# Kernel tuning notes

Hardware: AMD Instinct MI355X
Metric: run time of the kernel (lower is better)

## Reference

```python
import jax, jax.numpy as jnp
import numpy as np

RRELU_SLOPE = (1.0 / 8.0 + 1.0 / 3.0) / 2.0  # F.rrelu eval-mode slope = 11/48

N_NODES = 50000
N_EDGES = 800000
H_DIM = 128
N_REL2 = 460  # 2 * num_rels
T_DIM = 64
BATCH = 1024
SEQ_LEN = 10


def _rrelu(x):
    return jnp.where(x >= 0, x, x * RRELU_SLOPE)


def _rgcn_layer(h, rel, src, dst, etype, norm, has_in, w_neigh, loop_w, evolve_w):
    # UnionRGCNLayer (comp='sub'): msg = (h_src - rel[etype]) @ W_neigh, sum into dst, * 1/indeg
    msg = (h[src] - rel[etype]) @ w_neigh                                # [E, h]
    agg = jax.ops.segment_sum(msg, dst, num_segments=h.shape[0]) * norm  # [N, h]
    # self-loop: nodes with in-degree>0 use loop_weight, isolated nodes use evolve_loop_weight
    loop_msg = jnp.where(has_in[:, None], h @ loop_w, h @ evolve_w)
    return _rrelu(agg + loop_msg)  # dropout p=0.0 -> identity


def setup_inputs() -> dict:
    key = jax.random.key(0)
    ks = jax.random.split(key, 12)
    sc = 1.0 / np.sqrt(H_DIM)
    return {
        "h": jax.random.normal(ks[0], (N_NODES, H_DIM), jnp.float32),
        "rel_embeds": jax.random.normal(ks[1], (N_REL2, H_DIM), jnp.float32),
        "w_neigh1": jax.random.normal(ks[2], (H_DIM, H_DIM), jnp.float32) * sc,
        "loop_w1": jax.random.normal(ks[3], (H_DIM, H_DIM), jnp.float32) * sc,
        "evolve_w1": jax.random.normal(ks[4], (H_DIM, H_DIM), jnp.float32) * sc,
        "w_neigh2": jax.random.normal(ks[5], (H_DIM, H_DIM), jnp.float32) * sc,
        "loop_w2": jax.random.normal(ks[6], (H_DIM, H_DIM), jnp.float32) * sc,
        "evolve_w2": jax.random.normal(ks[7], (H_DIM, H_DIM), jnp.float32) * sc,
        "t_w": jax.random.normal(ks[8], (T_DIM,), jnp.float32),
        "t_b": jax.random.normal(ks[9], (T_DIM,), jnp.float32),
        "src": jax.random.randint(ks[10], (N_EDGES,), 0, N_NODES, jnp.int32),
        "dst": jax.random.randint(ks[11], (N_EDGES,), 0, N_NODES, jnp.int32),
        "etype": jax.random.randint(jax.random.fold_in(key, 1), (N_EDGES,), 0, N_REL2, jnp.int32),
        "node_ids_graph": jax.random.randint(jax.random.fold_in(key, 2), (BATCH, SEQ_LEN), 0, N_NODES + 1, jnp.int32),
        "times": jax.random.randint(jax.random.fold_in(key, 3), (BATCH, SEQ_LEN), 0, 1000, jnp.int32),
    }


def reference(h, rel_embeds, w_neigh1, loop_w1, evolve_w1, w_neigh2, loop_w2, evolve_w2,
              t_w, t_b, src, dst, etype, node_ids_graph, times):
    N, H = h.shape
    deg = jax.ops.segment_sum(jnp.ones_like(dst, dtype=h.dtype), dst, num_segments=N)
    has_in = deg > 0
    norm = (1.0 / jnp.maximum(deg, 1.0))[:, None]  # dgl 'norm' = 1/in-degree

    h1 = _rgcn_layer(h, rel_embeds, src, dst, etype, norm, has_in, w_neigh1, loop_w1, evolve_w1)
    h2 = _rgcn_layer(h1, rel_embeds, src, dst, etype, norm, has_in, w_neigh2, loop_w2, evolve_w2)

    # concat zero padding row, then irregular gather by node_ids_graph
    embeds = jnp.concatenate([h2, jnp.zeros((1, H), h.dtype)], axis=0)  # [N+1, h]
    s_embed = embeds[node_ids_graph]                                    # [B, L, h]

    B, L = node_ids_graph.shape
    t = times.reshape(-1, 1).astype(h.dtype)                            # [B*L, 1]
    time_emb = jnp.cos(t * t_w + t_b).reshape(B, L, t_w.shape[0])       # [B, L, t_dim]

    return jnp.concatenate([s_embed, time_emb], axis=-1)  # dropout p=0.0 -> identity
```

## Files before the change

kernel.cpp:

```cpp
#include <hip/hip_runtime.h>


#define HD 128
#define TD 64
#define BSH 7
#define NBLK 256
constexpr float SLOPE = 11.0f / 48.0f;

typedef unsigned short u16;
typedef unsigned int u32;
typedef short bf16x8 __attribute__((ext_vector_type(8)));
typedef float f32x4 __attribute__((ext_vector_type(4)));

__device__ __forceinline__ float bf2f(u16 b) {
    return __uint_as_float(((u32)b) << 16);
}
__device__ __forceinline__ u16 f2bf(float f) {
    u32 u = __float_as_uint(f);
    u += 0x7FFFu + ((u >> 16) & 1u);
    return (u16)(u >> 16);
}

__global__ __launch_bounds__(256)
void conv_kernel(const float4* __restrict__ in, ushort4* __restrict__ out, int n4)
{
    int i = blockIdx.x * 256 + threadIdx.x;
    if (i >= n4) return;
    float4 v = in[i];
    ushort4 o;
    o.x = f2bf(v.x); o.y = f2bf(v.y); o.z = f2bf(v.z); o.w = f2bf(v.w);
    out[i] = o;
}

__global__ __launch_bounds__(256)
void bt_kernel(const float* __restrict__ Wn, const float* __restrict__ Lw,
               u16* __restrict__ BT)
{
    int idx = blockIdx.x * 256 + threadIdx.x;
    int c = idx >> 8, k = idx & 255;
    float v = (k < HD) ? Wn[k * HD + c] : Lw[(k - HD) * HD + c];
    BT[(size_t)c * 256 + k] = f2bf(v);
}

__global__ __launch_bounds__(256)
void cntA(const int* __restrict__ dst, int E, int* __restrict__ cnt, int NBKT)
{
    __shared__ int hist[512];
    const int b = blockIdx.x, t = threadIdx.x;
    for (int i = t; i < NBKT; i += 256) hist[i] = 0;
    __syncthreads();
    const int chunk = (E + NBLK - 1) / NBLK;
    const int e0 = b * chunk;
    const int e1 = (e0 + chunk < E) ? e0 + chunk : E;
    for (int e = e0 + t; e < e1; e += 256)
        atomicAdd(&hist[dst[e] >> BSH], 1);
    __syncthreads();
    for (int i = t; i < NBKT; i += 256)
        cnt[(size_t)i * NBLK + b] = hist[i];
}

__global__ __launch_bounds__(256)
void scan1_kernel(const int* __restrict__ v, int* __restrict__ bsum, int M)
{
    __shared__ int red[256];
    const int b = blockIdx.x, t = threadIdx.x;
    int s = 0;
    #pragma unroll
    for (int j = 0; j < 4; j++) {
        int i = b * 1024 + j * 256 + t;
        if (i < M) s += v[i];
    }
    red[t] = s;
    __syncthreads();
    for (int off = 128; off; off >>= 1) {
        if (t < off) red[t] += red[t + off];
        __syncthreads();
    }
    if (t == 0) bsum[b] = red[0];
}

__global__ __launch_bounds__(64)
void scan2_kernel(int* __restrict__ bsum, int NB, int* __restrict__ totalOut)
{
    if (threadIdx.x == 0 && blockIdx.x == 0) {
        int acc = 0;
        for (int b = 0; b < NB; b++) { int x = bsum[b]; bsum[b] = acc; acc += x; }
        *totalOut = acc;
    }
}

__global__ __launch_bounds__(1024)
void scan3_kernel(const int* __restrict__ v, const int* __restrict__ bsum,
                  int* __restrict__ start, int M)
{
    __shared__ int buf[1024];
    const int b = blockIdx.x, t = threadIdx.x;
    const int i = b * 1024 + t;
    const int x = (i < M) ? v[i] : 0;
    buf[t] = x;
    __syncthreads();
    for (int off = 1; off < 1024; off <<= 1) {
        int y = (t >= off) ? buf[t - off] : 0;
        __syncthreads();
        buf[t] += y;
        __syncthreads();
    }
    if (i < M) start[i] = bsum[b] + buf[t] - x;
}

__global__ __launch_bounds__(256)
void passA2(const int* __restrict__ src, const int* __restrict__ dst,
            const int* __restrict__ ety, const int* __restrict__ start,
            u32* __restrict__ elistA, int E, int NBKT)
{
    __shared__ int cur[512];
    const int b = blockIdx.x, t = threadIdx.x;
    for (int i = t; i < NBKT; i += 256) cur[i] = start[(size_t)i * NBLK + b];
    __syncthreads();
    const int chunk = (E + NBLK - 1) / NBLK;
    const int e0 = b * chunk;
    const int e1 = (e0 + chunk < E) ? e0 + chunk : E;
    for (int e = e0 + t; e < e1; e += 256) {
        int d = dst[e];
        u32 entry = ((u32)(d & 127) << 25) | ((u32)ety[e] << 16) | (u32)src[e];
        int pos = atomicAdd(&cur[d >> BSH], 1);
        elistA[pos] = entry;
    }
}

__global__ __launch_bounds__(256)
void passB(const u32* __restrict__ elistA, const int* __restrict__ start,
           u32* __restrict__ elist, int* __restrict__ rowstart, int Nn, int E,
           int NBKT)
{
    __shared__ int cnt[128];
    __shared__ int ofs[128];
    const int b = blockIdx.x, t = threadIdx.x;
    const int beg = start[(size_t)b * NBLK];
    const int end = (b + 1 < NBKT) ? start[(size_t)(b + 1) * NBLK] : E;
    if (t < 128) cnt[t] = 0;
    __syncthreads();
    for (int i = beg + t; i < end; i += 256)
        atomicAdd(&cnt[elistA[i] >> 25], 1);
    __syncthreads();
    if (t == 0) {
        int acc = 0;
        for (int j = 0; j < 128; j++) { ofs[j] = acc; acc += cnt[j]; }
    }
    __syncthreads();
    const int n0 = b << BSH;
    if (t < 128 && n0 + t < Nn) rowstart[n0 + t] = beg + ofs[t];
    if (b == 0 && t == 0) rowstart[Nn] = E;
    __syncthreads();
    for (int i = beg + t; i < end; i += 256) {
        u32 v = elistA[i];
        int p = atomicAdd(&ofs[v >> 25], 1);
        elist[beg + p] = v & 0x01ffffffu;
    }
}

__global__ __launch_bounds__(64)
void gagg_kernel(const u32* __restrict__ hbf2, const u32* __restrict__ relbf2,
                 const u32* __restrict__ elist, const int* __restrict__ rowstart,
                 u32* __restrict__ Sn2, int Nn)
{
    int n = blockIdx.x;
    if (n >= Nn) return;
    int c = threadIdx.x;
    int beg = rowstart[n], end = rowstart[n + 1];
    float ae[8] = {}, ao[8] = {};
    int i = beg;
    for (; i + 8 <= end; i += 8) {
        #pragma unroll
        for (int j = 0; j < 8; j++) {
            u32 v = elist[i + j];
            u32 hv = hbf2[(size_t)(v & 0xffffu) * 64 + c];
            u32 rv = relbf2[(size_t)(v >> 16) * 64 + c];
            ae[j] += bf2f((u16)(hv & 0xffffu)) - bf2f((u16)(rv & 0xffffu));
            ao[j] += bf2f((u16)(hv >> 16)) - bf2f((u16)(rv >> 16));
        }
    }
    for (; i < end; i++) {
        u32 v = elist[i];
        u32 hv = hbf2[(size_t)(v & 0xffffu) * 64 + c];
        u32 rv = relbf2[(size_t)(v >> 16) * 64 + c];
        ae[0] += bf2f((u16)(hv & 0xffffu)) - bf2f((u16)(rv & 0xffffu));
        ao[0] += bf2f((u16)(hv >> 16)) - bf2f((u16)(rv >> 16));
    }
    float se = ((ae[0] + ae[1]) + (ae[2] + ae[3])) + ((ae[4] + ae[5]) + (ae[6] + ae[7]));
    float so = ((ao[0] + ao[1]) + (ao[2] + ao[3])) + ((ao[4] + ao[5]) + (ao[6] + ao[7]));
    int d = end - beg;
    float nrm = 1.0f / (float)((d > 0) ? d : 1);
    se *= nrm; so *= nrm;
    Sn2[(size_t)n * 64 + c] = (u32)f2bf(se) | ((u32)f2bf(so) << 16);
}

template<int STORE_BF16>
__global__ __launch_bounds__(256)
void mfma_kernel(const u16* __restrict__ Sn, const u16* __restrict__ Hn,
                 const u16* __restrict__ BT, const int* __restrict__ rowstart,
                 const float* __restrict__ Ew, void* __restrict__ Out, int Nn)
{
    const int lane = threadIdx.x & 63;
    const int wave = threadIdx.x >> 6;
    const int row0 = blockIdx.x * 128 + wave * 32;
    const int lr = lane & 15;
    const int lk = (lane >> 4) * 8;

    f32x4 acc[2][8];
    #pragma unroll
    for (int m = 0; m < 2; m++)
        #pragma unroll
        for (int n = 0; n < 8; n++)
            acc[m][n] = (f32x4){0.f, 0.f, 0.f, 0.f};

    int r0 = row0 + lr;      if (r0 >= Nn) r0 = Nn - 1;
    int r1 = row0 + 16 + lr; if (r1 >= Nn) r1 = Nn - 1;
    const size_t rb0 = (size_t)r0 * HD, rb1 = (size_t)r1 * HD;

    #pragma unroll
    for (int ks = 0; ks < 8; ks++) {
        const u16* A = (ks < 4) ? Sn : Hn;
        const int kc = (ks & 3) * 32 + lk;
        bf16x8 a0 = *(const bf16x8*)&A[rb0 + kc];
        bf16x8 a1 = *(const bf16x8*)&A[rb1 + kc];
        #pragma unroll
        for (int nf = 0; nf < 8; nf++) {
            bf16x8 b = *(const bf16x8*)&BT[(size_t)(nf * 16 + lr) * 256 + ks * 32 + lk];
            acc[0][nf] = __builtin_amdgcn_mfma_f32_16x16x32_bf16(a0, b, acc[0][nf], 0, 0, 0);
            acc[1][nf] = __builtin_amdgcn_mfma_f32_16x16x32_bf16(a1, b, acc[1][nf], 0, 0, 0);
        }
    }

    #pragma unroll
    for (int mf = 0; mf < 2; mf++) {
        #pragma unroll
        for (int r = 0; r < 4; r++) {
            const int row = row0 + mf * 16 + (lane >> 4) * 4 + r;
            if (row >= Nn) continue;
            const int d = rowstart[row + 1] - rowstart[row];
            #pragma unroll
            for (int nf = 0; nf < 8; nf++) {
                const int col = nf * 16 + lr;
                float o = acc[mf][nf][r];
                if (d == 0) {
                    o = 0.f;
                    for (int k = 0; k < HD; k++)
                        o = fmaf(bf2f(Hn[(size_t)row * HD + k]), Ew[(size_t)k * HD + col], o);
                }
                o = (o >= 0.f) ? o : o * SLOPE;
                if (STORE_BF16) ((u16*)Out)[(size_t)row * HD + col] = f2bf(o);
                else            ((float*)Out)[(size_t)row * HD + col] = o;
            }
        }
    }
}

__global__ __launch_bounds__(192)
void out_kernel(const float* __restrict__ h2, const int* __restrict__ ids,
                const int* __restrict__ tms,
                const float* __restrict__ tw, const float* __restrict__ tb,
                float* __restrict__ out, int R, int Nn)
{
    int r = blockIdx.x;
    int c = threadIdx.x;
    if (r >= R) return;
    float v;
    if (c < HD) {
        int id = ids[r];
        v = (id >= 0 && id < Nn) ? h2[(size_t)id * HD + c] : 0.0f;
    } else {
        int j = c - HD;
        v = cosf((float)tms[r] * tw[j] + tb[j]);
    }
    out[(size_t)r * (HD + TD) + c] = v;
}

extern "C" void kernel_launch(void* const* d_in, const int* in_sizes, int n_in,
                              void* d_out, int out_size, void* d_ws, size_t ws_size,
                              hipStream_t stream)
{
    const float* h   = (const float*)d_in[0];
    const float* rel = (const float*)d_in[1];
    const float* wn1 = (const float*)d_in[2];
    const float* lw1 = (const float*)d_in[3];
    const float* ew1 = (const float*)d_in[4];
    const float* wn2 = (const float*)d_in[5];
    const float* lw2 = (const float*)d_in[6];
    const float* ew2 = (const float*)d_in[7];
    const float* tw  = (const float*)d_in[8];
    const float* tb  = (const float*)d_in[9];
    const int* src = (const int*)d_in[10];
    const int* dst = (const int*)d_in[11];
    const int* ety = (const int*)d_in[12];
    const int* ids = (const int*)d_in[13];
    const int* tms = (const int*)d_in[14];

    const int Nn  = in_sizes[0] / HD;
    const int E   = in_sizes[10];
    const int R   = in_sizes[13];
    const int NR2 = in_sizes[1] / HD;
    const int NBKT = (Nn + 127) >> BSH;
    const int M = NBKT * NBLK;
    const int NBS = (M + 1023) / 1024;

    char* ws = (char*)d_ws;
    const size_t cntB  = ((size_t)M * 4 + 255) & ~(size_t)255;
    const size_t bsB   = ((size_t)NBS * 4 + 255) & ~(size_t)255;
    const size_t stB   = (((size_t)M + 1) * 4 + 255) & ~(size_t)255;
    const size_t rsB   = (((size_t)Nn + 1) * 4 + 255) & ~(size_t)255;
    int* cnt      = (int*)(ws);
    int* bsum     = (int*)(ws + cntB);
    int* start    = (int*)(ws + cntB + bsB);
    int* rowstart = (int*)(ws + cntB + bsB + stB);
    char* p       = ws + cntB + bsB + stB + rsB;
    u32* elistA = (u32*)p;   p += ((size_t)E * 4 + 255) & ~(size_t)255;
    u32* elist  = (u32*)p;   p += ((size_t)E * 4 + 255) & ~(size_t)255;
    u16* hbf    = (u16*)p;   p += (size_t)Nn * HD * 2;
    u16* h1bf   = (u16*)p;   p += (size_t)Nn * HD * 2;
    u16* Sn     = (u16*)p;   p += (size_t)Nn * HD * 2;
    float* h2   = (float*)p; p += (size_t)Nn * HD * 4;
    u16* relbf  = (u16*)p;   p += ((size_t)NR2 * HD * 2 + 255) & ~(size_t)255;
    u16* BT1    = (u16*)p;   p += HD * 256 * 2;
    u16* BT2    = (u16*)p;

    const int n4 = Nn * HD / 4;
    const int r4 = NR2 * HD / 4;
    const int gb = (Nn + 127) / 128;

    conv_kernel<<<(n4 + 255) / 256, 256, 0, stream>>>((const float4*)h, (ushort4*)hbf, n4);
    conv_kernel<<<(r4 + 255) / 256, 256, 0, stream>>>((const float4*)rel, (ushort4*)relbf, r4);
    bt_kernel<<<128, 256, 0, stream>>>(wn1, lw1, BT1);
    bt_kernel<<<128, 256, 0, stream>>>(wn2, lw2, BT2);

    cntA<<<NBLK, 256, 0, stream>>>(dst, E, cnt, NBKT);
    scan1_kernel<<<NBS, 256, 0, stream>>>(cnt, bsum, M);
    scan2_kernel<<<1, 64, 0, stream>>>(bsum, NBS, &start[M]);
    scan3_kernel<<<NBS, 1024, 0, stream>>>(cnt, bsum, start, M);
    passA2<<<NBLK, 256, 0, stream>>>(src, dst, ety, start, elistA, E, NBKT);
    passB<<<NBKT, 256, 0, stream>>>(elistA, start, elist, rowstart, Nn, E, NBKT);

    gagg_kernel<<<Nn, 64, 0, stream>>>((const u32*)hbf, (const u32*)relbf,
                                       elist, rowstart, (u32*)Sn, Nn);
    mfma_kernel<1><<<gb, 256, 0, stream>>>(Sn, hbf, BT1, rowstart, ew1, h1bf, Nn);

    gagg_kernel<<<Nn, 64, 0, stream>>>((const u32*)h1bf, (const u32*)relbf,
                                       elist, rowstart, (u32*)Sn, Nn);
    mfma_kernel<0><<<gb, 256, 0, stream>>>(Sn, h1bf, BT2, rowstart, ew2, h2, Nn);

    out_kernel<<<R, 192, 0, stream>>>(h2, ids, tms, tw, tb, (float*)d_out, R, Nn);
}
```

Measured before the change: 172.6 us.

## Stage weight tile in swizzled LDS and store final layer output as bf16

Each mfma block now copies the 128x256 bf16 weight matrix into shared memory with an XOR swizzle, then reads B fragments from LDS instead of global memory. The second layer output is written as bf16 rather than fp32, and the output gather converts it back to float. This is meant to cut global and L2 traffic for weight reads and halve h2 write and read bytes. In exchange, it uses 64KB of LDS per block, which may limit occupancy, and it loses precision in the final embeddings.

```diff
diff --git a/kernel.cpp b/kernel.cpp
--- a/kernel.cpp
+++ b/kernel.cpp
@@ -195,14 +195,26 @@
     Sn2[(size_t)n * 64 + c] = (u32)f2bf(se) | ((u32)f2bf(so) << 16);
 }
 
-template<int STORE_BF16>
 __global__ __launch_bounds__(256)
 void mfma_kernel(const u16* __restrict__ Sn, const u16* __restrict__ Hn,
                  const u16* __restrict__ BT, const int* __restrict__ rowstart,
-                 const float* __restrict__ Ew, void* __restrict__ Out, int Nn)
-{
-    const int lane = threadIdx.x & 63;
-    const int wave = threadIdx.x >> 6;
+                 const float* __restrict__ Ew, u16* __restrict__ Out, int Nn)
+{
+    __shared__ u16 BTs[128 * 256];
+
+    const int tid = threadIdx.x;
+    #pragma unroll
+    for (int j = 0; j < 16; j++) {
+        int chunk = tid + j * 256;
+        int byte = chunk << 4;
+        int row = byte >> 9;
+        int sw = byte ^ ((row & 7) << 4);
+        *(ulonglong2*)((char*)BTs + sw) = *(const ulonglong2*)((const char*)BT + byte);
+    }
+    __syncthreads();
+
+    const int lane = tid & 63;
+    const int wave = tid >> 6;
     const int row0 = blockIdx.x * 128 + wave * 32;
     const int lr = lane & 15;
     const int lk = (lane >> 4) * 8;
@@ -226,7 +238,10 @@
         bf16x8 a1 = *(const bf16x8*)&A[rb1 + kc];
         #pragma unroll
         for (int nf = 0; nf < 8; nf++) {
-            bf16x8 b = *(const bf16x8*)&BT[(size_t)(nf * 16 + lr) * 256 + ks * 32 + lk];
+            const int brow = nf * 16 + lr;
+            int boff = (brow << 9) + ((ks * 32 + lk) << 1);
+            boff ^= (brow & 7) << 4;
+            bf16x8 b = *(const bf16x8*)((const char*)BTs + boff);
             acc[0][nf] = __builtin_amdgcn_mfma_f32_16x16x32_bf16(a0, b, acc[0][nf], 0, 0, 0);
             acc[1][nf] = __builtin_amdgcn_mfma_f32_16x16x32_bf16(a1, b, acc[1][nf], 0, 0, 0);
         }
@@ -249,15 +264,14 @@
                         o = fmaf(bf2f(Hn[(size_t)row * HD + k]), Ew[(size_t)k * HD + col], o);
                 }
                 o = (o >= 0.f) ? o : o * SLOPE;
-                if (STORE_BF16) ((u16*)Out)[(size_t)row * HD + col] = f2bf(o);
-                else            ((float*)Out)[(size_t)row * HD + col] = o;
+                Out[(size_t)row * HD + col] = f2bf(o);
             }
         }
     }
 }
 
 __global__ __launch_bounds__(192)
-void out_kernel(const float* __restrict__ h2, const int* __restrict__ ids,
+void out_kernel(const u16* __restrict__ h2, const int* __restrict__ ids,
                 const int* __restrict__ tms,
                 const float* __restrict__ tw, const float* __restrict__ tb,
                 float* __restrict__ out, int R, int Nn)
@@ -268,7 +282,7 @@
     float v;
     if (c < HD) {
         int id = ids[r];
-        v = (id >= 0 && id < Nn) ? h2[(size_t)id * HD + c] : 0.0f;
+        v = (id >= 0 && id < Nn) ? bf2f(h2[(size_t)id * HD + c]) : 0.0f;
     } else {
         int j = c - HD;
         v = cosf((float)tms[r] * tw[j] + tb[j]);
@@ -319,7 +333,7 @@
     u16* hbf    = (u16*)p;   p += (size_t)Nn * HD * 2;
     u16* h1bf   = (u16*)p;   p += (size_t)Nn * HD * 2;
     u16* Sn     = (u16*)p;   p += (size_t)Nn * HD * 2;
-    float* h2   = (float*)p; p += (size_t)Nn * HD * 4;
+    u16* h2bf   = (u16*)p;   p += (size_t)Nn * HD * 2;
     u16* relbf  = (u16*)p;   p += ((size_t)NR2 * HD * 2 + 255) & ~(size_t)255;
     u16* BT1    = (u16*)p;   p += HD * 256 * 2;
     u16* BT2    = (u16*)p;
@@ -342,11 +356,11 @@
 
     gagg_kernel<<<Nn, 64, 0, stream>>>((const u32*)hbf, (const u32*)relbf,
                                        elist, rowstart, (u32*)Sn, Nn);
-    mfma_kernel<1><<<gb, 256, 0, stream>>>(Sn, hbf, BT1, rowstart, ew1, h1bf, Nn);
+    mfma_kernel<<<gb, 256, 0, stream>>>(Sn, hbf, BT1, rowstart, ew1, h1bf, Nn);
 
     gagg_kernel<<<Nn, 64, 0, stream>>>((const u32*)h1bf, (const u32*)relbf,
                                        elist, rowstart, (u32*)Sn, Nn);
-    mfma_kernel<0><<<gb, 256, 0, stream>>>(Sn, h1bf, BT2, rowstart, ew2, h2, Nn);
-
-    out_kernel<<<R, 192, 0, stream>>>(h2, ids, tms, tw, tb, (float*)d_out, R, Nn);
-}
+    mfma_kernel<<<gb, 256, 0, stream>>>(Sn, h1bf, BT2, rowstart, ew2, h2bf, Nn);
+
+    out_kernel<<<R, 192, 0, stream>>>(h2bf, ids, tms, tw, tb, (float*)d_out, R, Nn);
+}
```

Result: faster. 148.6 us (-13.9%).
